# Kernel optimization log

Hardware: AMD Instinct MI355X
Metric: run time of the kernel (lower is better)

Reference implementation:

```python
import jax, jax.numpy as jnp
import numpy as np

NEG = -9999.0      # chart init / clip floor (np.clip a_min=-9999.0)
THRESH = -9000.0   # 'pseudo_score > -9000' acceptance gate
ARC_BONUS = 5.0    # '+ 5' added to every arc candidate


def _fill_chart(vinfo):
    """Eisner DP chart fill, faithful to the sequential numpy triple loop.
    vinfo: [N, N] arc scores. Returns (score_chart [N,N,2,2], backtrace [N,N,2,2]).
    Chart axes: [i, j, direction, completeness] as in the torch source.
    Parallelized over span start i and split q; sequential over width k via scan.
    Sequential-update subtleties of the original q-loop are reproduced exactly:
      * complete (0,1) at q=i reads the (0,0) cell as it stands after only the
        q=i incomplete update ('part00');
      * complete (1,1) at q=j reads the fully updated (1,0) cell ('new10');
      * complete (0,1) at q=j and (1,1) at q=i are strict-improvement no-ops;
      * ties keep the earliest q (jnp.argmax returns first occurrence).
    """
    N = vinfo.shape[0]
    idx = jnp.arange(N)
    ii = idx[:, None]   # span start i
    mm = idx[None, :]   # split offset m; q = i + m
    S = jnp.full((N, N, 2, 2), NEG, dtype=vinfo.dtype).at[idx, idx].set(0.0)
    BT = jnp.zeros((N, N, 2, 2), dtype=jnp.int32)

    def step(carry, k):
        S, BT = carry
        j = idx + k
        row_ok = j < N
        okb = row_ok[:, None]
        jc = jnp.minimum(j, N - 1)
        jb = jc[:, None]
        q = ii + mm
        qc = jnp.minimum(q, N - 1)
        q1c = jnp.minimum(q + 1, N - 1)

        # ---- incomplete spans (0,0) and (1,0): q in [i, j-1]  <=>  m in [0, k-1]
        base = jnp.where((mm < k) & okb,
                         S[:, :, 1, 1][ii, qc] + S[:, :, 0, 1][q1c, jb],
                         -jnp.inf)                      # [N (i), N (m)]
        vL = vinfo[jc, idx][:, None]   # vinfo[j, i] -> arc j<-...: head j
        vR = vinfo[idx, jc][:, None]   # vinfo[i, j]
        p00 = jnp.maximum(base + vL + ARC_BONUS, NEG)
        p10 = jnp.maximum(base + vR + ARC_BONUS, NEG)
        m00 = jnp.max(p00, axis=1); q00 = idx + jnp.argmax(p00, axis=1)
        m10 = jnp.max(p10, axis=1); q10 = idx + jnp.argmax(p10, axis=1)
        ok00 = row_ok & (m00 > THRESH)
        ok10 = row_ok & (m10 > THRESH)
        # chart[i,j,0,0] as it stands right after the q=i iteration
        part00 = jnp.where(row_ok & (p00[:, 0] > THRESH), p00[:, 0], NEG)
        new10 = jnp.where(ok10, m10, NEG)

        m_mid = (mm >= 1) & (mm < k) & okb
        # ---- complete (0,1): q=i uses partially built (0,0); q=j is a no-op
        c01 = jnp.where(m_mid, S[:, :, 0, 1][ii, qc] + S[:, :, 0, 0][qc, jb], -jnp.inf)
        c01 = c01.at[:, 0].set(jnp.where(row_ok, part00, -jnp.inf))
        p01 = jnp.maximum(c01, NEG)
        m01 = jnp.max(p01, axis=1); q01 = idx + jnp.argmax(p01, axis=1)
        ok01 = row_ok & (m01 > THRESH)

        # ---- complete (1,1): q=i is a no-op; q=j uses freshly updated (1,0)
        c11 = jnp.where(m_mid, S[:, :, 1, 0][ii, qc] + S[:, :, 1, 1][qc, jb], -jnp.inf)
        c11 = jnp.where((mm == k) & okb, new10[:, None], c11)
        p11 = jnp.maximum(c11, NEG)
        m11 = jnp.max(p11, axis=1); q11 = idx + jnp.argmax(p11, axis=1)
        ok11 = row_ok & (m11 > THRESH)

        def upd(S, BT, a, b, ok, val, qarg):
            S = S.at[idx, jc, a, b].set(jnp.where(ok, val, S[idx, jc, a, b]))
            BT = BT.at[idx, jc, a, b].set(
                jnp.where(ok, qarg, BT[idx, jc, a, b]).astype(jnp.int32))
            return S, BT

        S, BT = upd(S, BT, 0, 0, ok00, m00, q00)
        S, BT = upd(S, BT, 1, 0, ok10, m10, q10)
        S, BT = upd(S, BT, 0, 1, ok01, m01, q01)
        S, BT = upd(S, BT, 1, 1, ok11, m11, q11)
        return (S, BT), None

    (S, BT), _ = jax.lax.scan(step, (S, BT), jnp.arange(1, N))
    return S, BT


def setup_inputs() -> dict:
    key = jax.random.key(0)
    B, N = 64, 128
    b_vinfo_mtx = jax.random.normal(key, (B, N, N), dtype=jnp.float32)
    b_buffer_size = jnp.full((B,), N, dtype=jnp.int32)
    return {"b_vinfo_mtx": b_vinfo_mtx, "b_buffer_size": b_buffer_size}


def reference(b_vinfo_mtx, b_buffer_size):
    # All sentences use the full buffer (b_buffer_size == N), so the batch is
    # processed as one vmapped chart fill.
    scores, backtrace = jax.vmap(_fill_chart)(b_vinfo_mtx)
    return scores, backtrace
```

## Files before the change

### kernel.cpp

```cpp
#include <hip/hip_runtime.h>
#include <stdint.h>

static constexpr int kN = 128;
static constexpr int kTri = (kN * (kN - 1)) / 2;
static constexpr int kTriD = (kN * (kN + 1)) / 2;
static constexpr int kThreads = 1024;
static constexpr float kNeg = -9999.0f;
static constexpr float kThresh = -9000.0f;
static constexpr float kArcBonus = 5.0f;
static constexpr int kDynLds = kTriD * 16;
static constexpr int kCMax = 9;

__device__ __forceinline__ int rowBase(int i) { return (i * (2 * kN - 1 - i)) / 2; }
__device__ __forceinline__ int colBaseD(int c) { return (c * (c + 1)) / 2; }

__device__ __forceinline__ void ldsBarrier() {
    asm volatile("s_waitcnt lgkmcnt(0)\n\ts_barrier" ::: "memory");
}

template <int CTRL>
__device__ __forceinline__ float dppMax(float x) {
    const int y = __builtin_amdgcn_update_dpp(__float_as_int(x), __float_as_int(x),
                                              CTRL, 0xF, 0xF, true);
    return fmaxf(x, __int_as_float(y));
}
template <int CTRL>
__device__ __forceinline__ int dppMinI(int x) {
    const int y = __builtin_amdgcn_update_dpp(x, x, CTRL, 0xF, 0xF, true);
    return (y < x) ? y : x;
}

__device__ __forceinline__ float4 writeCell(float4* __restrict__ Q4,
                                            uint32_t* __restrict__ wsBT,
                                            int qjb, int i, int wsIdx, int k,
                                            float gb, int ib, float vLc, float vRc,
                                            float v01, int i01, float v11, int i11) {
    const float v00 = (gb + vLc) + kArcBonus;
    const float v10 = (gb + vRc) + kArcBonus;
    const float new10 = (v10 > kThresh) ? v10 : kNeg;
    if (new10 > v11) { v11 = new10; i11 = k; }
    float4 w = make_float4(kNeg, kNeg, kNeg, kNeg);
    uint32_t p = 0;
    if (v00 > kThresh) { w.x = v00; p |= (uint32_t)(i + ib); }
    if (v01 > kThresh) { w.z = v01; p |= (uint32_t)(i + i01) << 8; }
    if (v10 > kThresh) { w.w = v10; p |= (uint32_t)(i + ib) << 16; }
    if (v11 > kThresh) { w.y = v11; p |= (uint32_t)(i + i11) << 24; }
    Q4[qjb + i] = w;
    wsBT[wsIdx] = p;
    return w;
}

__device__ __forceinline__ void doStepSerialReg(int k, int i,
                                                float4* __restrict__ Q4,
                                                uint32_t* __restrict__ wsBT,
                                                int& j, int& qjb, int rbi,
                                                const float*& pL, const float*& pR,
                                                float& vL, float& vR,
                                                float (&sr11)[17], float (&sr01)[17],
                                                float (&sr10)[17]) {
    const bool act = i < kN - k;
    const float vLc = vL, vRc = vR;
    const int jc = j, qjbc = qjb;
    float bmax = -3.0e38f, v01 = -3.0e38f, v11 = -3.0e38f;
    int ib = 0, i01 = 0, i11 = 0x7FFFFFFF;
    if (act) {
        float4 cur = Q4[qjbc + i + 1];
        bmax = cur.z; ib = 0;
        const float p00 = (cur.z + vLc) + kArcBonus;
        v01 = (p00 > kThresh) ? p00 : kNeg; i01 = 0;
#pragma unroll
        for (int m = 1; m < 16; ++m) {
            if (m < k) {
                const float4 nxt = Q4[qjbc + i + m + 1];
                const float base = sr11[m] + nxt.z;
                const float p01v = sr01[m] + cur.x;
                const float p11v = sr10[m] + cur.y;
                if (base > bmax) { bmax = base; ib = m; }
                if (p01v > v01) { v01 = p01v; i01 = m; }
                if (p11v > v11) { v11 = p11v; i11 = m; }
                cur = nxt;
            }
        }
    }
    if (k < 16) {
        const bool nact = i < kN - (k + 1);
        qjb += j + 1; ++j; pL += kN; ++pR;
        vL = nact ? *pL : 0.f;
        vR = nact ? *pR : 0.f;
    }
    if (act) {
        const float4 w = writeCell(Q4, wsBT, qjbc, i, rbi + k - 1, k,
                                   bmax, ib, vLc, vRc, v01, i01, v11, i11);
        sr11[k] = w.y; sr01[k] = w.z; sr10[k] = w.w;
    }
    (void)jc;
}

template <int LP, int C>
__device__ __forceinline__ void preloadRow(int k0, int tid,
                                           const float4* __restrict__ Q4,
                                           float (&r11)[kCMax], float (&r01)[kCMax],
                                           float (&r10)[kCMax]) {
    constexpr int P = 1 << LP;
    const int i = tid >> LP;
    const int l = tid & (P - 1);
    const int mlo = l * C;
    const int mstart = mlo ? mlo : 1;
    const bool act = i < (kN - k0);
#pragma unroll
    for (int c = 0; c < C; ++c) {
        const int m = mstart + c;
        if (act && (m < mlo + C) && (m <= k0 - 1)) {
            const float4 d = Q4[colBaseD(i + m) + i];
            r11[c] = d.y; r01[c] = d.z; r10[c] = d.w;
        }
    }
}

template <int LP, int C>
__device__ __forceinline__ void fwInit(int k0, int tid,
                                       const float (&r11)[kCMax], const float (&r01)[kCMax],
                                       const float (&r10)[kCMax],
                                       float& fw11, float& fw01, float& fw10) {
    constexpr int P = 1 << LP;
    const int l = tid & (P - 1);
    const int mlo = l * C;
    const int mstart = mlo ? mlo : 1;
#pragma unroll
    for (int c = 0; c < C; ++c) {
        if (mstart + c == k0 - 1) { fw11 = r11[c]; fw01 = r01[c]; fw10 = r10[c]; }
    }
}

template <int LP, int C>
__device__ __forceinline__ void doStepC(int k, int i, int l, int tid,
                                        float4* __restrict__ Q4,
                                        uint32_t* __restrict__ wsBT,
                                        int& j, int& qjb, int rbi,
                                        const float*& pL, const float*& pR,
                                        float& vL, float& vR,
                                        float (&r11)[kCMax], float (&r01)[kCMax],
                                        float (&r10)[kCMax],
                                        float& fw11, float& fw01, float& fw10) {
    constexpr int P = 1 << LP;
    static_assert(P <= 16, "reductions must stay pure-DPP");
    const bool act = i < kN - k;
    const float vLc = vL, vRc = vR;
    const int mlo = l * C;
    const int mstart = mlo ? mlo : 1;
    const int mhi = (mlo + C < k) ? (mlo + C) : k;
    const bool waveActive = (((tid & ~63) >> LP) < (kN - k));
    const int qjbc = qjb;

    float bmax = -3.0e38f, v01 = -3.0e38f, v11 = -3.0e38f;
    int ib = 0x7FFFFFFF, i01 = 0x7FFFFFFF, i11 = 0x7FFFFFFF;

    const int mf = k - 1;
    const bool lact = waveActive && act && (mstart < mhi);
    float4 cur = make_float4(0.f, 0.f, 0.f, 0.f);
    if (lact) cur = Q4[qjbc + i + mstart];
    if (act && mlo == 0) {
        bmax = cur.z; ib = 0;
        const float p00 = (cur.z + vLc) + kArcBonus;
        v01 = (p00 > kThresh) ? p00 : kNeg; i01 = 0;
    }
#pragma unroll
    for (int c = 0; c < C; ++c) {
        const int m = mstart + c;
        const bool isF = (m == mf);
        const float a11 = isF ? fw11 : r11[c];
        const float a01 = isF ? fw01 : r01[c];
        const float a10 = isF ? fw10 : r10[c];
        r11[c] = a11; r01[c] = a01; r10[c] = a10;
        const bool on = lact && (m < mhi);
        if (on) {
            const float4 nxt = Q4[qjbc + i + m + 1];
            const float base = a11 + nxt.z;
            const float p01v = a01 + cur.x;
            const float p11v = a10 + cur.y;
            if (base > bmax) { bmax = base; ib = m; }
            if (p01v > v01) { v01 = p01v; i01 = m; }
            if (p11v > v11) { v11 = p11v; i11 = m; }
            cur = nxt;
        }
    }

    {
        const bool nact = i < kN - (k + 1);
        qjb += j + 1; ++j; pL += kN; ++pR;
        vL = nact ? *pL : 0.f;
        vR = nact ? *pR : 0.f;
    }

    if (waveActive) {
        float gB = dppMax<0x141>(dppMax<0x4E>(dppMax<0xB1>(bmax)));
        float g01 = dppMax<0x141>(dppMax<0x4E>(dppMax<0xB1>(v01)));
        float g11 = dppMax<0x141>(dppMax<0x4E>(dppMax<0xB1>(v11)));
        if constexpr (P == 16) {
            gB = dppMax<0x140>(gB); g01 = dppMax<0x140>(g01); g11 = dppMax<0x140>(g11);
        }
        int cB = (bmax == gB) ? ib : 0x7FFFFFFF;
        int c01 = (v01 == g01) ? i01 : 0x7FFFFFFF;
        int c11 = (v11 == g11) ? i11 : 0x7FFFFFFF;
        cB = dppMinI<0x141>(dppMinI<0x4E>(dppMinI<0xB1>(cB)));
        c01 = dppMinI<0x141>(dppMinI<0x4E>(dppMinI<0xB1>(c01)));
        c11 = dppMinI<0x141>(dppMinI<0x4E>(dppMinI<0xB1>(c11)));
        if constexpr (P == 16) {
            cB = dppMinI<0x140>(cB); c01 = dppMinI<0x140>(c01); c11 = dppMinI<0x140>(c11);
        }

        const float v10f = (gB + vRc) + kArcBonus;
        const float new10 = (v10f > kThresh) ? v10f : kNeg;
        float v11m = g11;
        if (new10 > v11m) v11m = new10;
        fw11 = (v11m > kThresh) ? v11m : kNeg;
        fw01 = (g01 > kThresh) ? g01 : kNeg;
        fw10 = (v10f > kThresh) ? v10f : kNeg;

        if (act && l == 0) {
            writeCell(Q4, wsBT, qjbc, i, rbi + k - 1, k,
                      gB, cB, vLc, vRc, g01, c01, g11, c11);
        }
    }
}

template <int LP, int C>
__device__ __forceinline__ void runPhaseC(int k0, int k1, int tid,
        float4* __restrict__ Q4, uint32_t* __restrict__ wsBT,
        const float* __restrict__ v,
        float (&r11)[kCMax], float (&r01)[kCMax], float (&r10)[kCMax]) {
    constexpr int P = 1 << LP;
    const int i = tid >> LP;
    const int l = tid & (P - 1);
    int j = i + k0;
    int qjb = colBaseD(j);
    const int rbi = rowBase(i & (kN - 1));
    const float* pL = v + (size_t)j * kN + i;
    const float* pR = v + (size_t)i * kN + j;
    const bool a0 = i < kN - k0;
    float vL = a0 ? *pL : 0.f;
    float vR = a0 ? *pR : 0.f;
    preloadRow<LP, C>(k0, tid, Q4, r11, r01, r10);
    float fw11 = kNeg, fw01 = kNeg, fw10 = kNeg;
    fwInit<LP, C>(k0, tid, r11, r01, r10, fw11, fw01, fw10);
    for (int k = k0; k < k1; ++k) {
        doStepC<LP, C>(k, i, l, tid, Q4, wsBT, j, qjb, rbi, pL, pR, vL, vR,
                       r11, r01, r10, fw11, fw01, fw10);
        ldsBarrier();
    }
}

__global__ __launch_bounds__(kThreads) void eisner_dp(
    const float* __restrict__ vinfo,
    float* __restrict__ outS,
    float* __restrict__ outBT,
    uint32_t* __restrict__ btPacked)
{
    extern __shared__ float4 Q4[];

    const int tid = threadIdx.x;
    const int b = blockIdx.x;
    const float* v = vinfo + (size_t)b * kN * kN;
    uint32_t* wsBT = btPacked + (size_t)b * kTri;

    const float4 zeroq = make_float4(0.f, 0.f, 0.f, 0.f);
    if (tid < kN) Q4[colBaseD(tid) + tid] = zeroq;
    __syncthreads();

    {
        const int i = tid;
        float sr11[17], sr01[17], sr10[17];
        int j = i + 1;
        int qjb = colBaseD(j);
        const int rbi = rowBase(i & (kN - 1));
        const float* pL = v + (size_t)j * kN + i;
        const float* pR = v + (size_t)i * kN + j;
        const bool a0 = i < kN - 1;
        float vL = a0 ? *pL : 0.f;
        float vR = a0 ? *pR : 0.f;
#pragma unroll
        for (int k = 1; k <= 16; ++k) {
            doStepSerialReg(k, i, Q4, wsBT, j, qjb, rbi, pL, pR, vL, vR,
                            sr11, sr01, sr10);
            ldsBarrier();
        }
    }

    float r11[kCMax], r01[kCMax], r10[kCMax];
#pragma unroll
    for (int c = 0; c < kCMax; ++c) { r11[c] = kNeg; r01[c] = kNeg; r10[c] = kNeg; }

    runPhaseC<3, 3>(17, 24, tid, Q4, wsBT, v, r11, r01, r10);
    runPhaseC<3, 5>(24, 40, tid, Q4, wsBT, v, r11, r01, r10);
    runPhaseC<3, 7>(40, 56, tid, Q4, wsBT, v, r11, r01, r10);
    runPhaseC<3, 9>(56, 64, tid, Q4, wsBT, v, r11, r01, r10);
    runPhaseC<4, 5>(64, 80, tid, Q4, wsBT, v, r11, r01, r10);
    runPhaseC<4, 7>(80, 112, tid, Q4, wsBT, v, r11, r01, r10);
    runPhaseC<4, 9>(112, 128, tid, Q4, wsBT, v, r11, r01, r10);

    __syncthreads();

    float4* gS4 = (float4*)(outS + (size_t)b * kN * kN * 4);
    float4* gB4 = (float4*)(outBT + (size_t)b * kN * kN * 4);
    const float4 negq = make_float4(kNeg, kNeg, kNeg, kNeg);
    for (int c = tid; c < kN * kN; c += kThreads) {
        const int i = c >> 7, j = c & (kN - 1);
        if (i < j) {
            const float4 q = Q4[colBaseD(j) + i];
            gS4[c] = make_float4(q.x, q.z, q.w, q.y);
            const uint32_t p = wsBT[rowBase(i) + (j - i - 1)];
            gB4[c] = make_float4((float)(p & 255u), (float)((p >> 8) & 255u),
                                 (float)((p >> 16) & 255u), (float)(p >> 24));
        } else if (i == j) {
            gS4[c] = zeroq;
            gB4[c] = zeroq;
        } else {
            gS4[c] = negq;
            gB4[c] = zeroq;
        }
    }
}

extern "C" void kernel_launch(void* const* d_in, const int* in_sizes, int n_in,
                              void* d_out, int out_size, void* d_ws, size_t ws_size,
                              hipStream_t stream) {
    (void)n_in; (void)out_size; (void)ws_size;
    const float* vinfo = (const float*)d_in[0];
    const int B = in_sizes[1];
    float* outS = (float*)d_out;
    float* outBT = outS + (size_t)B * kN * kN * 4;
    uint32_t* btPacked = (uint32_t*)d_ws;

    hipFuncSetAttribute(reinterpret_cast<const void*>(eisner_dp),
                        hipFuncAttributeMaxDynamicSharedMemorySize, kDynLds);

    eisner_dp<<<dim3(B), dim3(kThreads), kDynLds, stream>>>(vinfo, outS, outBT, btPacked);
}
```

Baseline: 230.5 us.

## Halve block to 512 threads, retune per-span split schedule and skip idle waves

```diff
diff --git a/kernel.cpp b/kernel.cpp
--- a/kernel.cpp
+++ b/kernel.cpp
@@ -4,12 +4,12 @@
 static constexpr int kN = 128;
 static constexpr int kTri = (kN * (kN - 1)) / 2;
 static constexpr int kTriD = (kN * (kN + 1)) / 2;
-static constexpr int kThreads = 1024;
+static constexpr int kThreads = 512;
 static constexpr float kNeg = -9999.0f;
 static constexpr float kThresh = -9000.0f;
 static constexpr float kArcBonus = 5.0f;
 static constexpr int kDynLds = kTriD * 16;
-static constexpr int kCMax = 9;
+static constexpr int kCMax = 16;
 
 __device__ __forceinline__ int rowBase(int i) { return (i * (2 * kN - 1 - i)) / 2; }
 __device__ __forceinline__ int colBaseD(int c) { return (c * (c + 1)) / 2; }
@@ -60,7 +60,7 @@
                                                 float (&sr10)[17]) {
     const bool act = i < kN - k;
     const float vLc = vL, vRc = vR;
-    const int jc = j, qjbc = qjb;
+    const int qjbc = qjb;
     float bmax = -3.0e38f, v01 = -3.0e38f, v11 = -3.0e38f;
     int ib = 0, i01 = 0, i11 = 0x7FFFFFFF;
     if (act) {
@@ -93,7 +93,6 @@
                                    bmax, ib, vLc, vRc, v01, i01, v11, i11);
         sr11[k] = w.y; sr01[k] = w.z; sr10[k] = w.w;
     }
-    (void)jc;
 }
 
 template <int LP, int C>
@@ -101,9 +100,8 @@
                                            const float4* __restrict__ Q4,
                                            float (&r11)[kCMax], float (&r01)[kCMax],
                                            float (&r10)[kCMax]) {
-    constexpr int P = 1 << LP;
     const int i = tid >> LP;
-    const int l = tid & (P - 1);
+    const int l = tid & ((1 << LP) - 1);
     const int mlo = l * C;
     const int mstart = mlo ? mlo : 1;
     const bool act = i < (kN - k0);
@@ -122,8 +120,7 @@
                                        const float (&r11)[kCMax], const float (&r01)[kCMax],
                                        const float (&r10)[kCMax],
                                        float& fw11, float& fw01, float& fw10) {
-    constexpr int P = 1 << LP;
-    const int l = tid & (P - 1);
+    const int l = tid & ((1 << LP) - 1);
     const int mlo = l * C;
     const int mstart = mlo ? mlo : 1;
 #pragma unroll
@@ -133,7 +130,7 @@
 }
 
 template <int LP, int C>
-__device__ __forceinline__ void doStepC(int k, int i, int l, int tid,
+__device__ __forceinline__ void doStepC(int k, int i, int l,
                                         float4* __restrict__ Q4,
                                         uint32_t* __restrict__ wsBT,
                                         int& j, int& qjb, int rbi,
@@ -143,20 +140,19 @@
                                         float (&r10)[kCMax],
                                         float& fw11, float& fw01, float& fw10) {
     constexpr int P = 1 << LP;
-    static_assert(P <= 16, "reductions must stay pure-DPP");
+    static_assert(P <= 8, "reductions are 2-3 DPP levels");
     const bool act = i < kN - k;
     const float vLc = vL, vRc = vR;
     const int mlo = l * C;
     const int mstart = mlo ? mlo : 1;
     const int mhi = (mlo + C < k) ? (mlo + C) : k;
-    const bool waveActive = (((tid & ~63) >> LP) < (kN - k));
     const int qjbc = qjb;
 
     float bmax = -3.0e38f, v01 = -3.0e38f, v11 = -3.0e38f;
     int ib = 0x7FFFFFFF, i01 = 0x7FFFFFFF, i11 = 0x7FFFFFFF;
 
     const int mf = k - 1;
-    const bool lact = waveActive && act && (mstart < mhi);
+    const bool lact = act && (mstart < mhi);
     float4 cur = make_float4(0.f, 0.f, 0.f, 0.f);
     if (lact) cur = Q4[qjbc + i + mstart];
     if (act && mlo == 0) {
@@ -192,35 +188,33 @@
         vR = nact ? *pR : 0.f;
     }
 
-    if (waveActive) {
-        float gB = dppMax<0x141>(dppMax<0x4E>(dppMax<0xB1>(bmax)));
-        float g01 = dppMax<0x141>(dppMax<0x4E>(dppMax<0xB1>(v01)));
-        float g11 = dppMax<0x141>(dppMax<0x4E>(dppMax<0xB1>(v11)));
-        if constexpr (P == 16) {
-            gB = dppMax<0x140>(gB); g01 = dppMax<0x140>(g01); g11 = dppMax<0x140>(g11);
-        }
-        int cB = (bmax == gB) ? ib : 0x7FFFFFFF;
-        int c01 = (v01 == g01) ? i01 : 0x7FFFFFFF;
-        int c11 = (v11 == g11) ? i11 : 0x7FFFFFFF;
-        cB = dppMinI<0x141>(dppMinI<0x4E>(dppMinI<0xB1>(cB)));
-        c01 = dppMinI<0x141>(dppMinI<0x4E>(dppMinI<0xB1>(c01)));
-        c11 = dppMinI<0x141>(dppMinI<0x4E>(dppMinI<0xB1>(c11)));
-        if constexpr (P == 16) {
-            cB = dppMinI<0x140>(cB); c01 = dppMinI<0x140>(c01); c11 = dppMinI<0x140>(c11);
-        }
-
-        const float v10f = (gB + vRc) + kArcBonus;
-        const float new10 = (v10f > kThresh) ? v10f : kNeg;
-        float v11m = g11;
-        if (new10 > v11m) v11m = new10;
-        fw11 = (v11m > kThresh) ? v11m : kNeg;
-        fw01 = (g01 > kThresh) ? g01 : kNeg;
-        fw10 = (v10f > kThresh) ? v10f : kNeg;
-
-        if (act && l == 0) {
-            writeCell(Q4, wsBT, qjbc, i, rbi + k - 1, k,
-                      gB, cB, vLc, vRc, g01, c01, g11, c11);
-        }
+    float gB = dppMax<0x4E>(dppMax<0xB1>(bmax));
+    float g01 = dppMax<0x4E>(dppMax<0xB1>(v01));
+    float g11 = dppMax<0x4E>(dppMax<0xB1>(v11));
+    if constexpr (P == 8) {
+        gB = dppMax<0x141>(gB); g01 = dppMax<0x141>(g01); g11 = dppMax<0x141>(g11);
+    }
+    int cB = (bmax == gB) ? ib : 0x7FFFFFFF;
+    int c01 = (v01 == g01) ? i01 : 0x7FFFFFFF;
+    int c11 = (v11 == g11) ? i11 : 0x7FFFFFFF;
+    cB = dppMinI<0x4E>(dppMinI<0xB1>(cB));
+    c01 = dppMinI<0x4E>(dppMinI<0xB1>(c01));
+    c11 = dppMinI<0x4E>(dppMinI<0xB1>(c11));
+    if constexpr (P == 8) {
+        cB = dppMinI<0x141>(cB); c01 = dppMinI<0x141>(c01); c11 = dppMinI<0x141>(c11);
+    }
+
+    const float v10f = (gB + vRc) + kArcBonus;
+    const float new10 = (v10f > kThresh) ? v10f : kNeg;
+    float v11m = g11;
+    if (new10 > v11m) v11m = new10;
+    fw11 = (v11m > kThresh) ? v11m : kNeg;
+    fw01 = (g01 > kThresh) ? g01 : kNeg;
+    fw10 = (v10f > kThresh) ? v10f : kNeg;
+
+    if (act && l == 0) {
+        writeCell(Q4, wsBT, qjbc, i, rbi + k - 1, k,
+                  gB, cB, vLc, vRc, g01, c01, g11, c11);
     }
 }
 
@@ -229,24 +223,31 @@
         float4* __restrict__ Q4, uint32_t* __restrict__ wsBT,
         const float* __restrict__ v,
         float (&r11)[kCMax], float (&r01)[kCMax], float (&r10)[kCMax]) {
-    constexpr int P = 1 << LP;
     const int i = tid >> LP;
-    const int l = tid & (P - 1);
-    int j = i + k0;
-    int qjb = colBaseD(j);
-    const int rbi = rowBase(i & (kN - 1));
-    const float* pL = v + (size_t)j * kN + i;
-    const float* pR = v + (size_t)i * kN + j;
-    const bool a0 = i < kN - k0;
-    float vL = a0 ? *pL : 0.f;
-    float vR = a0 ? *pR : 0.f;
-    preloadRow<LP, C>(k0, tid, Q4, r11, r01, r10);
-    float fw11 = kNeg, fw01 = kNeg, fw10 = kNeg;
-    fwInit<LP, C>(k0, tid, r11, r01, r10, fw11, fw01, fw10);
-    for (int k = k0; k < k1; ++k) {
-        doStepC<LP, C>(k, i, l, tid, Q4, wsBT, j, qjb, rbi, pL, pR, vL, vR,
-                       r11, r01, r10, fw11, fw01, fw10);
-        ldsBarrier();
+    const int l = tid & ((1 << LP) - 1);
+    const int firstGroup = (tid & ~63) >> LP;
+    int kEnd = kN - firstGroup;
+    if (kEnd > k1) kEnd = k1;
+    if (kEnd > k0) {
+        int j = i + k0;
+        int qjb = colBaseD(j);
+        const int rbi = rowBase(i & (kN - 1));
+        const float* pL = v + (size_t)j * kN + i;
+        const float* pR = v + (size_t)i * kN + j;
+        const bool a0 = i < kN - k0;
+        float vL = a0 ? *pL : 0.f;
+        float vR = a0 ? *pR : 0.f;
+        preloadRow<LP, C>(k0, tid, Q4, r11, r01, r10);
+        float fw11 = kNeg, fw01 = kNeg, fw10 = kNeg;
+        fwInit<LP, C>(k0, tid, r11, r01, r10, fw11, fw01, fw10);
+        for (int k = k0; k < kEnd; ++k) {
+            doStepC<LP, C>(k, i, l, Q4, wsBT, j, qjb, rbi, pL, pR, vL, vR,
+                           r11, r01, r10, fw11, fw01, fw10);
+            ldsBarrier();
+        }
+        for (int k = kEnd; k < k1; ++k) ldsBarrier();
+    } else {
+        for (int k = k0; k < k1; ++k) ldsBarrier();
     }
 }
 
@@ -267,7 +268,7 @@
     if (tid < kN) Q4[colBaseD(tid) + tid] = zeroq;
     __syncthreads();
 
-    {
+    if ((tid & ~63) < kN - 1) {
         const int i = tid;
         float sr11[17], sr01[17], sr10[17];
         int j = i + 1;
@@ -284,19 +285,20 @@
                             sr11, sr01, sr10);
             ldsBarrier();
         }
+    } else {
+#pragma unroll
+        for (int k = 1; k <= 16; ++k) ldsBarrier();
     }
 
     float r11[kCMax], r01[kCMax], r10[kCMax];
 #pragma unroll
     for (int c = 0; c < kCMax; ++c) { r11[c] = kNeg; r01[c] = kNeg; r10[c] = kNeg; }
 
-    runPhaseC<3, 3>(17, 24, tid, Q4, wsBT, v, r11, r01, r10);
-    runPhaseC<3, 5>(24, 40, tid, Q4, wsBT, v, r11, r01, r10);
-    runPhaseC<3, 7>(40, 56, tid, Q4, wsBT, v, r11, r01, r10);
-    runPhaseC<3, 9>(56, 64, tid, Q4, wsBT, v, r11, r01, r10);
-    runPhaseC<4, 5>(64, 80, tid, Q4, wsBT, v, r11, r01, r10);
-    runPhaseC<4, 7>(80, 112, tid, Q4, wsBT, v, r11, r01, r10);
-    runPhaseC<4, 9>(112, 128, tid, Q4, wsBT, v, r11, r01, r10);
+    runPhaseC<2, 8>(17, 32, tid, Q4, wsBT, v, r11, r01, r10);
+    runPhaseC<2, 12>(32, 48, tid, Q4, wsBT, v, r11, r01, r10);
+    runPhaseC<2, 16>(48, 64, tid, Q4, wsBT, v, r11, r01, r10);
+    runPhaseC<3, 12>(64, 96, tid, Q4, wsBT, v, r11, r01, r10);
+    runPhaseC<3, 16>(96, 128, tid, Q4, wsBT, v, r11, r01, r10);
 
     __syncthreads();
 
```

After: 282.5 us. 1.23x slower.
